# Optimization experiments

Measured on AMD Instinct MI355X. Metric: run time of the kernel, lower is better.

The kernel has to match this reference:

```python
import jax, jax.numpy as jnp
import numpy as np
import math

DIM = 4096
BATCH = 8192
SCALE = 1.0 / math.sqrt(DIM)


def fwht(x):
    """Fast Walsh-Hadamard Transform along last axis (iterative butterfly).
    Faithful to the torch reshape/slice/cat implementation; the Python while
    loop is over log2(n) static stages, fine under jit.
    """
    n = x.shape[-1]
    h = 1
    while h < n:
        x = x.reshape(*x.shape[:-1], n // (2 * h), 2 * h)
        a = x[..., :h]
        b = x[..., h:]
        x = jnp.concatenate([a + b, a - b], axis=-1)
        x = x.reshape(*x.shape[:-2], n)
        h *= 2
    return x


def setup_inputs() -> dict:
    key = jax.random.key(0)
    kx, k1, k2, k3, k4 = jax.random.split(key, 5)
    x = jax.random.normal(kx, (BATCH, DIM), dtype=jnp.float32)
    # +/-1 random sign diagonals
    d1 = (jax.random.randint(k1, (DIM,), 0, 2).astype(jnp.float32) * 2 - 1)
    d2 = (jax.random.randint(k2, (DIM,), 0, 2).astype(jnp.float32) * 2 - 1)
    # |N(0,1)| gaussian diagonal
    gauss_d = jnp.abs(jax.random.normal(k3, (DIM,), dtype=jnp.float32))
    # random permutation of [0, DIM)
    perm = jax.random.permutation(k4, DIM).astype(jnp.int64)
    return {"x": x, "d1": d1, "d2": d2, "gauss_d": gauss_d, "perm": perm}


def reference(x, d1, d2, gauss_d, perm):
    # W ~= D2 @ H @ G @ Pi @ H @ D1, applied to each row of x
    y = x * d1
    y = fwht(y)
    y = y[..., perm]
    y = y * gauss_d
    y = fwht(y)
    y = y * d2
    return y * SCALE
```

## Files before the change

### kernel.cpp

```cpp
#include <hip/hip_runtime.h>

#define DIM 4096
#define FF_SCALE 0.015625f

__device__ __forceinline__ int pad(int i) { return i + ((i >> 6) << 2); }

__device__ __forceinline__ void fwht16(float v[16]) {
#pragma unroll
    for (int h = 1; h < 16; h <<= 1) {
#pragma unroll
        for (int i = 0; i < 16; ++i) {
            if ((i & h) == 0) {
                float a = v[i], b = v[i + h];
                v[i] = a + b;
                v[i + h] = a - b;
            }
        }
    }
}

template <int CTRL>
__device__ __forceinline__ float qperm(float x) {
    return __int_as_float(
        __builtin_amdgcn_mov_dpp(__float_as_int(x), CTRL, 0xF, 0xF, true));
}

template <int CTRL>
__device__ __forceinline__ void qbutterfly(float v[16], float s) {
#pragma unroll
    for (int e = 0; e < 16; ++e) {
        float p = qperm<CTRL>(v[e]);
        v[e] = fmaf(v[e], s, p);
    }
}

__global__ __launch_bounds__(256, 8) void fastfood_kernel(
    const float* __restrict__ x,
    const float* __restrict__ d1,
    const float* __restrict__ d2,
    const float* __restrict__ gauss_d,
    const int* __restrict__ perm,
    float* __restrict__ out)
{
    __shared__ float lds[64 * 68];
    const int t = threadIdx.x;
    const float s1 = (t & 1) ? -1.f : 1.f;
    const float s2 = (t & 2) ? -1.f : 1.f;
    const size_t rowoff = (size_t)blockIdx.x * DIM;

    const int aBase = 16 * t + ((t >> 2) << 2);
    const int bBase = (t >> 2) + 1088 * (t & 3);

    float v[16];

    {
        const float4* xv = (const float4*)(x + rowoff + t * 16);
        const float4* dv = (const float4*)(d1 + t * 16);
#pragma unroll
        for (int q = 0; q < 4; ++q) {
            float4 a = xv[q], d = dv[q];
            v[4 * q + 0] = a.x * d.x;
            v[4 * q + 1] = a.y * d.y;
            v[4 * q + 2] = a.z * d.z;
            v[4 * q + 3] = a.w * d.w;
        }
    }

    fwht16(v);
    qbutterfly<0xB1>(v, s1);
    qbutterfly<0x4E>(v, s2);
#pragma unroll
    for (int q = 0; q < 4; ++q)
        *(float4*)(lds + aBase + 4 * q) =
            make_float4(v[4 * q], v[4 * q + 1], v[4 * q + 2], v[4 * q + 3]);
    __syncthreads();

#pragma unroll
    for (int g = 0; g < 4; ++g) {
        const int bg = bBase + 272 * g;
#pragma unroll
        for (int m = 0; m < 4; ++m) v[4 * g + m] = lds[bg + 68 * m];
    }
    fwht16(v);
    qbutterfly<0xB1>(v, s1);
    qbutterfly<0x4E>(v, s2);
#pragma unroll
    for (int g = 0; g < 4; ++g) {
        const int bg = bBase + 272 * g;
#pragma unroll
        for (int m = 0; m < 4; ++m) lds[bg + 68 * m] = v[4 * g + m];
    }
    __syncthreads();

    {
        const int4* pv = (const int4*)(perm + t * 16);
        const float4* gv = (const float4*)(gauss_d + t * 16);
#pragma unroll
        for (int q = 0; q < 4; ++q) {
            int4 p4 = pv[q];
            float4 g4 = gv[q];
            v[4 * q + 0] = lds[pad(p4.x)] * g4.x;
            v[4 * q + 1] = lds[pad(p4.y)] * g4.y;
            v[4 * q + 2] = lds[pad(p4.z)] * g4.z;
            v[4 * q + 3] = lds[pad(p4.w)] * g4.w;
        }
    }

    fwht16(v);
    qbutterfly<0xB1>(v, s1);
    qbutterfly<0x4E>(v, s2);
    __syncthreads();
#pragma unroll
    for (int q = 0; q < 4; ++q)
        *(float4*)(lds + aBase + 4 * q) =
            make_float4(v[4 * q], v[4 * q + 1], v[4 * q + 2], v[4 * q + 3]);
    __syncthreads();

#pragma unroll
    for (int g = 0; g < 4; ++g) {
        const int bg = bBase + 272 * g;
#pragma unroll
        for (int m = 0; m < 4; ++m) v[4 * g + m] = lds[bg + 68 * m];
    }
    fwht16(v);
    qbutterfly<0xB1>(v, s1);
    qbutterfly<0x4E>(v, s2);
    {
        const int B = (t >> 2) + ((t & 3) << 10);
        const float* d2p = d2 + B;
        float* op = out + rowoff + B;
#pragma unroll
        for (int c = 0; c < 16; ++c)
            op[64 * c] = (v[c] * d2p[64 * c]) * FF_SCALE;
    }
}

extern "C" void kernel_launch(void* const* d_in, const int* in_sizes, int n_in,
                              void* d_out, int out_size, void* d_ws, size_t ws_size,
                              hipStream_t stream) {
    const float* x       = (const float*)d_in[0];
    const float* d1      = (const float*)d_in[1];
    const float* d2      = (const float*)d_in[2];
    const float* gauss_d = (const float*)d_in[3];
    const int*   perm    = (const int*)d_in[4];
    float* out = (float*)d_out;

    const int batch = in_sizes[0] / DIM;
    fastfood_kernel<<<batch, 256, 0, stream>>>(x, d1, d2, gauss_d, perm, out);
}
```

Baseline: 256.7 us.

## Replace DPP quad butterflies with three-pass LDS radix-16 FWHT using packed fp32 math

Each FWHT is now done as three radix-16 passes through LDS instead of two radix-16 passes plus two DPP cross-lane butterfly stages per transform. The butterflies use v_pk_add/v_pk_mul inline asm to halve VALU instruction count, and the scale is folded into gauss_d. This adds an extra LDS round trip and barrier per transform, with new padding (every 256 elements), in exchange for removing the DPP movs and FMAs. Output stores become fully coalesced with stride-1 lanes.

```diff
diff --git a/kernel.cpp b/kernel.cpp
--- a/kernel.cpp
+++ b/kernel.cpp
@@ -3,36 +3,45 @@
 #define DIM 4096
 #define FF_SCALE 0.015625f
 
-__device__ __forceinline__ int pad(int i) { return i + ((i >> 6) << 2); }
+typedef __attribute__((ext_vector_type(2))) float f32x2;
 
-__device__ __forceinline__ void fwht16(float v[16]) {
+__device__ __forceinline__ f32x2 pk_add(f32x2 a, f32x2 b) {
+    f32x2 d;
+    asm("v_pk_add_f32 %0, %1, %2" : "=v"(d) : "v"(a), "v"(b));
+    return d;
+}
+__device__ __forceinline__ f32x2 pk_sub(f32x2 a, f32x2 b) {
+    f32x2 d;
+    asm("v_pk_add_f32 %0, %1, %2 neg_lo:[0,1] neg_hi:[0,1]"
+        : "=v"(d) : "v"(a), "v"(b));
+    return d;
+}
+__device__ __forceinline__ f32x2 pk_mul(f32x2 a, f32x2 b) {
+    f32x2 d;
+    asm("v_pk_mul_f32 %0, %1, %2" : "=v"(d) : "v"(a), "v"(b));
+    return d;
+}
+
+__device__ __forceinline__ void fwht16_pk(f32x2 p[8]) {
 #pragma unroll
-    for (int h = 1; h < 16; h <<= 1) {
+    for (int m = 0; m < 8; ++m) {
+        float a = p[m].x, b = p[m].y;
+        p[m].x = a + b;
+        p[m].y = a - b;
+    }
 #pragma unroll
-        for (int i = 0; i < 16; ++i) {
-            if ((i & h) == 0) {
-                float a = v[i], b = v[i + h];
-                v[i] = a + b;
-                v[i + h] = a - b;
+    for (int h2 = 1; h2 < 8; h2 <<= 1) {
+#pragma unroll
+        for (int m = 0; m < 8; ++m)
+            if ((m & h2) == 0) {
+                f32x2 a = p[m], b = p[m + h2];
+                p[m] = pk_add(a, b);
+                p[m + h2] = pk_sub(a, b);
             }
-        }
     }
 }
 
-template <int CTRL>
-__device__ __forceinline__ float qperm(float x) {
-    return __int_as_float(
-        __builtin_amdgcn_mov_dpp(__float_as_int(x), CTRL, 0xF, 0xF, true));
-}
-
-template <int CTRL>
-__device__ __forceinline__ void qbutterfly(float v[16], float s) {
-#pragma unroll
-    for (int e = 0; e < 16; ++e) {
-        float p = qperm<CTRL>(v[e]);
-        v[e] = fmaf(v[e], s, p);
-    }
-}
+__device__ __forceinline__ int padidx(int i) { return i + ((i >> 8) << 2); }
 
 __global__ __launch_bounds__(256, 8) void fastfood_kernel(
     const float* __restrict__ x,
@@ -42,53 +51,59 @@
     const int* __restrict__ perm,
     float* __restrict__ out)
 {
-    __shared__ float lds[64 * 68];
+    __shared__ float lds[DIM + 64];
     const int t = threadIdx.x;
-    const float s1 = (t & 1) ? -1.f : 1.f;
-    const float s2 = (t & 2) ? -1.f : 1.f;
     const size_t rowoff = (size_t)blockIdx.x * DIM;
 
-    const int aBase = 16 * t + ((t >> 2) << 2);
-    const int bBase = (t >> 2) + 1088 * (t & 3);
+    const int base_r1 = 16 * t + ((t >> 4) << 2);
+    const int base_r2 = 260 * (t >> 4) + (t & 15);
 
-    float v[16];
+    f32x2 p[8];
 
     {
         const float4* xv = (const float4*)(x + rowoff + t * 16);
         const float4* dv = (const float4*)(d1 + t * 16);
 #pragma unroll
         for (int q = 0; q < 4; ++q) {
-            float4 a = xv[q], d = dv[q];
-            v[4 * q + 0] = a.x * d.x;
-            v[4 * q + 1] = a.y * d.y;
-            v[4 * q + 2] = a.z * d.z;
-            v[4 * q + 3] = a.w * d.w;
+            float4 aa = xv[q], dd = dv[q];
+            p[2 * q]     = pk_mul((f32x2){aa.x, aa.y}, (f32x2){dd.x, dd.y});
+            p[2 * q + 1] = pk_mul((f32x2){aa.z, aa.w}, (f32x2){dd.z, dd.w});
         }
     }
 
-    fwht16(v);
-    qbutterfly<0xB1>(v, s1);
-    qbutterfly<0x4E>(v, s2);
+    fwht16_pk(p);
 #pragma unroll
-    for (int q = 0; q < 4; ++q)
-        *(float4*)(lds + aBase + 4 * q) =
-            make_float4(v[4 * q], v[4 * q + 1], v[4 * q + 2], v[4 * q + 3]);
+    for (int m = 0; m < 8; ++m)
+        *(f32x2*)(lds + base_r1 + 2 * m) = p[m];
     __syncthreads();
 
 #pragma unroll
-    for (int g = 0; g < 4; ++g) {
-        const int bg = bBase + 272 * g;
+    for (int m = 0; m < 8; ++m) {
+        f32x2 w;
+        w.x = lds[base_r2 + 32 * m];
+        w.y = lds[base_r2 + 32 * m + 16];
+        p[m] = w;
+    }
+    fwht16_pk(p);
 #pragma unroll
-        for (int m = 0; m < 4; ++m) v[4 * g + m] = lds[bg + 68 * m];
+    for (int m = 0; m < 8; ++m) {
+        lds[base_r2 + 32 * m]      = p[m].x;
+        lds[base_r2 + 32 * m + 16] = p[m].y;
     }
-    fwht16(v);
-    qbutterfly<0xB1>(v, s1);
-    qbutterfly<0x4E>(v, s2);
+    __syncthreads();
+
 #pragma unroll
-    for (int g = 0; g < 4; ++g) {
-        const int bg = bBase + 272 * g;
+    for (int m = 0; m < 8; ++m) {
+        f32x2 w;
+        w.x = lds[t + 520 * m];
+        w.y = lds[t + 520 * m + 260];
+        p[m] = w;
+    }
+    fwht16_pk(p);
 #pragma unroll
-        for (int m = 0; m < 4; ++m) lds[bg + 68 * m] = v[4 * g + m];
+    for (int m = 0; m < 8; ++m) {
+        lds[t + 520 * m]       = p[m].x;
+        lds[t + 520 * m + 260] = p[m].y;
     }
     __syncthreads();
 
@@ -99,39 +114,60 @@
         for (int q = 0; q < 4; ++q) {
             int4 p4 = pv[q];
             float4 g4 = gv[q];
-            v[4 * q + 0] = lds[pad(p4.x)] * g4.x;
-            v[4 * q + 1] = lds[pad(p4.y)] * g4.y;
-            v[4 * q + 2] = lds[pad(p4.z)] * g4.z;
-            v[4 * q + 3] = lds[pad(p4.w)] * g4.w;
+            f32x2 lo, hi;
+            lo.x = lds[padidx(p4.x)];
+            lo.y = lds[padidx(p4.y)];
+            hi.x = lds[padidx(p4.z)];
+            hi.y = lds[padidx(p4.w)];
+            f32x2 gs0 = pk_mul((f32x2){g4.x, g4.y}, (f32x2){FF_SCALE, FF_SCALE});
+            f32x2 gs1 = pk_mul((f32x2){g4.z, g4.w}, (f32x2){FF_SCALE, FF_SCALE});
+            p[2 * q]     = pk_mul(lo, gs0);
+            p[2 * q + 1] = pk_mul(hi, gs1);
         }
     }
 
-    fwht16(v);
-    qbutterfly<0xB1>(v, s1);
-    qbutterfly<0x4E>(v, s2);
+    fwht16_pk(p);
     __syncthreads();
 #pragma unroll
-    for (int q = 0; q < 4; ++q)
-        *(float4*)(lds + aBase + 4 * q) =
-            make_float4(v[4 * q], v[4 * q + 1], v[4 * q + 2], v[4 * q + 3]);
+    for (int m = 0; m < 8; ++m)
+        *(f32x2*)(lds + base_r1 + 2 * m) = p[m];
     __syncthreads();
 
 #pragma unroll
-    for (int g = 0; g < 4; ++g) {
-        const int bg = bBase + 272 * g;
+    for (int m = 0; m < 8; ++m) {
+        f32x2 w;
+        w.x = lds[base_r2 + 32 * m];
+        w.y = lds[base_r2 + 32 * m + 16];
+        p[m] = w;
+    }
+    fwht16_pk(p);
 #pragma unroll
-        for (int m = 0; m < 4; ++m) v[4 * g + m] = lds[bg + 68 * m];
+    for (int m = 0; m < 8; ++m) {
+        lds[base_r2 + 32 * m]      = p[m].x;
+        lds[base_r2 + 32 * m + 16] = p[m].y;
     }
-    fwht16(v);
-    qbutterfly<0xB1>(v, s1);
-    qbutterfly<0x4E>(v, s2);
+    __syncthreads();
+
+#pragma unroll
+    for (int m = 0; m < 8; ++m) {
+        f32x2 w;
+        w.x = lds[t + 520 * m];
+        w.y = lds[t + 520 * m + 260];
+        p[m] = w;
+    }
+    fwht16_pk(p);
     {
-        const int B = (t >> 2) + ((t & 3) << 10);
-        const float* d2p = d2 + B;
-        float* op = out + rowoff + B;
+        const float* d2p = d2 + t;
+        float* op = out + rowoff + t;
 #pragma unroll
-        for (int c = 0; c < 16; ++c)
-            op[64 * c] = (v[c] * d2p[64 * c]) * FF_SCALE;
+        for (int m = 0; m < 8; ++m) {
+            f32x2 dd;
+            dd.x = d2p[512 * m];
+            dd.y = d2p[512 * m + 256];
+            f32x2 r = pk_mul(p[m], dd);
+            op[512 * m]       = r.x;
+            op[512 * m + 256] = r.y;
+        }
     }
 }
 
```

Measured after the change: 253.1 us. Within noise of the previous version (-1.4%).
